# Kernel tuning notes

Hardware: AMD Instinct MI355X
Metric: run time of the kernel (lower is better)

Reference implementation:

```python
import jax, jax.numpy as jnp
import numpy as np

N = 4096        # nodes
C = 256         # in_channels
E0 = 65536      # edges before adding self-loops
RATIO = 0.5
K = int(np.ceil(RATIO * N))   # pooled nodes (topk)
NEG = 0.2       # leaky relu negative slope


def setup_inputs() -> dict:
    key = jax.random.key(0)
    ks = jax.random.split(key, 12)
    x = jax.random.normal(ks[0], (N, C), jnp.float32)
    src = jax.random.randint(ks[1], (E0,), 0, N)
    off = jax.random.randint(ks[2], (E0,), 1, N)
    dst = (src + off) % N                      # guaranteed no self-loops
    edge_index = jnp.stack([src, dst]).astype(jnp.int32)
    s = 1.0 / np.sqrt(C)
    s2 = 1.0 / np.sqrt(2 * C)
    u = lambda k, shape, b: jax.random.uniform(k, shape, jnp.float32, -b, b)
    return dict(
        x=x, edge_index=edge_index,
        Wq=u(ks[3], (C, C), s), bq=u(ks[4], (C,), s),          # lin_q
        gat_w=u(ks[5], (2 * C,), s2), gat_b=u(ks[6], (1,), s2),  # gat_att
        le1_w=u(ks[7], (C,), s), le1_b=u(ks[8], (1,), s),      # LEConv lin1
        le2_w=u(ks[9], (C,), s),                                # LEConv lin2 (no bias)
        le3_w=u(ks[10], (C,), s), le3_b=u(ks[11], (1,), s),    # LEConv lin3
    )


def _asap(x, edge_index, Wq, bq, gat_w, gat_b, le1_w, le1_b, le2_w, le3_w, le3_b):
    # add_remaining_self_loops (inputs have none -> all N loops, weight 1)
    loops = jnp.arange(N, dtype=edge_index.dtype)
    ei = jnp.concatenate([edge_index, jnp.stack([loops, loops])], axis=1)
    i, j = ei[0], ei[1]          # i: aggregation target, j: neighbor

    x_pool = x                   # GNN is None -> x_pool = x
    xj = x_pool[j]               # [E, C]

    # Master2Token attention: X_q = scatter_max over target i
    Xq = jax.ops.segment_max(xj, i, num_segments=N)       # [N, C]
    Mq = Xq @ Wq + bq                                     # lin_q
    sc = jnp.concatenate([Mq[i], xj], axis=-1) @ gat_w + gat_b[0]  # [E]
    sc = jnp.where(sc > 0, sc, NEG * sc)                  # leaky relu

    # segment softmax over targets i
    m = jax.ops.segment_max(sc, i, num_segments=N)
    e = jnp.exp(sc - m[i])
    z = jax.ops.segment_sum(e, i, num_segments=N)
    score = e / z[i]                                      # dropout_att=0, eval

    # cluster representation
    out = jax.ops.segment_sum(x[j] * score[:, None], i, num_segments=N)  # [N, C]

    # fitness = sigmoid(LEConv(out)): x_i' = lin3(x_i) + sum_j (lin1(x_j) - lin2(x_i))
    a = out @ le1_w + le1_b[0]                            # [N]
    b = out @ le2_w                                       # [N]
    agg = jax.ops.segment_sum(a[j] - b[i], i, num_segments=N)
    fitness = jax.nn.sigmoid(agg + out @ le3_w + le3_b[0])  # [N]

    # topk pooling (single graph -> global top_k)
    fit_k, perm = jax.lax.top_k(fitness, K)
    x_out = out[perm] * fit_k[:, None]                    # [K, C]

    # graph_connectivity: E = S^T A S (dense stand-in for coalesce+spspmm)
    n_idx = jnp.zeros(N, jnp.int32).at[perm].set(jnp.arange(K, dtype=jnp.int32))
    in_perm = jnp.zeros(N, bool).at[perm].set(True)
    sS = jax.lax.stop_gradient(score) * in_perm[i]        # score.detach(), kept-cluster edges
    S = jnp.zeros((N, K), x.dtype).at[j, n_idx[i]].add(sS)   # S[j, new(i)] = score
    A = jnp.zeros((N, N), x.dtype).at[i, j].add(1.0)      # edge_weight None -> ones, coalesced
    Eadj = S.T @ (A @ S)                                  # [K, K]
    # remove_self_loops then add_remaining_self_loops(fill=1)
    Eadj = Eadj - jnp.diag(jnp.diag(Eadj)) + jnp.eye(K, dtype=Eadj.dtype)
    return x_out, Eadj, perm


def reference(x, edge_index, Wq, bq, gat_w, gat_b, le1_w, le1_b, le2_w, le3_w, le3_b):
    return _asap(x, edge_index, Wq, bq, gat_w, gat_b,
                 le1_w, le1_b, le2_w, le3_w, le3_b)
```

## Files before the change

kernel.cpp:

```cpp
#include <hip/hip_runtime.h>
#include <math.h>

constexpr int NN  = 4096;
constexpr int CC  = 256;
constexpr int EE0 = 65536;
constexpr int EE  = 69632;
constexpr int KK  = 2048;
constexpr int SL  = 128;

__device__ __forceinline__ void edge_ij(const int* __restrict__ ei, int e, int& i, int& j) {
    if (e < EE0) { i = ei[e]; j = ei[EE0 + e]; }
    else         { i = e - EE0; j = i; }
}
__device__ __forceinline__ int edge_i(const int* __restrict__ ei, int e) {
    return (e < EE0) ? ei[e] : e - EE0;
}
__device__ __forceinline__ int edge_j(const int* __restrict__ ei, int e) {
    return (e < EE0) ? ei[EE0 + e] : e - EE0;
}

__global__ __launch_bounds__(256) void k_build(const int* __restrict__ ei,
                                               int* cnt_i, int* cnt_j,
                                               int* lst_i, int* lst_j,
                                               const float* __restrict__ x,
                                               const float* __restrict__ Wq, const float* __restrict__ bq,
                                               const float* __restrict__ gat_w, const float* __restrict__ gat_b,
                                               double* wv, double* consts, double* beta_node, int EB) {
    const int t = threadIdx.x, g = t >> 6, l = t & 63;
    if ((int)blockIdx.x < EB) {
        int e = blockIdx.x * 256 + t;
        if (e >= EE) return;
        int i, j; edge_ij(ei, e, i, j);
        int si = atomicAdd(&cnt_i[i], 1);
        lst_i[i * SL + si] = e;
        int sj = atomicAdd(&cnt_j[j], 1);
        lst_j[j * SL + sj] = e;
        return;
    }
    if ((int)blockIdx.x < EB + CC) {
        int k = blockIdx.x - EB;
        double s = (double)Wq[k * CC + t] * (double)gat_w[t];
        #pragma unroll
        for (int d = 32; d > 0; d >>= 1) s += __shfl_down(s, d, 64);
        __shared__ double red[4];
        if (l == 0) red[g] = s;
        __syncthreads();
        if (t == 0) wv[k] = red[0] + red[1] + red[2] + red[3];
        if (k == 0 && t == 0) {
            double cb = 0.0;
            for (int q = 0; q < CC; ++q) cb += (double)bq[q] * (double)gat_w[q];
            consts[0] = cb + (double)gat_b[0];
        }
        return;
    }
    int m = (blockIdx.x - EB - CC) * 4 + g;
    const float* gw2 = gat_w + CC;
    float4 v = ((const float4*)(x + (size_t)m * CC))[l];
    double s = (double)v.x * (double)gw2[4 * l]     + (double)v.y * (double)gw2[4 * l + 1]
             + (double)v.z * (double)gw2[4 * l + 2] + (double)v.w * (double)gw2[4 * l + 3];
    #pragma unroll
    for (int d = 32; d > 0; d >>= 1) s += __shfl_down(s, d, 64);
    if (l == 0) beta_node[m] = s;
}

__global__ __launch_bounds__(256) void k_attn(const float* __restrict__ x, const int* __restrict__ ei,
                                              const int* __restrict__ cnt_i, const int* __restrict__ lst_i,
                                              const int* __restrict__ cnt_j, const int* __restrict__ lst_j,
                                              const double* __restrict__ wv, const double* __restrict__ beta_node,
                                              const double* __restrict__ consts,
                                              const float* __restrict__ le1_w, const float* __restrict__ le1_b,
                                              const float* __restrict__ le2_w,
                                              const float* __restrict__ le3_w, const float* __restrict__ le3_b,
                                              float* __restrict__ score32, float* __restrict__ out32,
                                              double* __restrict__ zlog) {
    __shared__ int    sj[SL];
    __shared__ double ssc[SL];
    __shared__ double mz[2];
    __shared__ double bcast;
    __shared__ union { float4 m4[4][64]; double d[4][CC]; } red;

    const int n = blockIdx.x, t = threadIdx.x, g = t >> 6, l = t & 63;
    const int base = n * SL;
    const int deg = cnt_i[n];

    for (int p = t; p < deg; p += 256) {
        int e = lst_i[base + p];
        int j = edge_j(ei, e);
        sj[p] = j;
        ssc[p] = beta_node[j];
    }
    __syncthreads();

    float4 mx = make_float4(-INFINITY, -INFINITY, -INFINITY, -INFINITY);
    for (int p = g; p < deg; p += 4) {
        float4 v = ((const float4*)(x + (size_t)sj[p] * CC))[l];
        mx.x = fmaxf(mx.x, v.x); mx.y = fmaxf(mx.y, v.y);
        mx.z = fmaxf(mx.z, v.z); mx.w = fmaxf(mx.w, v.w);
    }
    red.m4[g][l] = mx;
    __syncthreads();
    if (g == 0) {
        float4 a = red.m4[0][l], b = red.m4[1][l], c2 = red.m4[2][l], d4 = red.m4[3][l];
        float m0 = fmaxf(fmaxf(a.x, b.x), fmaxf(c2.x, d4.x));
        float m1 = fmaxf(fmaxf(a.y, b.y), fmaxf(c2.y, d4.y));
        float m2 = fmaxf(fmaxf(a.z, b.z), fmaxf(c2.z, d4.z));
        float m3 = fmaxf(fmaxf(a.w, b.w), fmaxf(c2.w, d4.w));
        double alph = (double)m0 * wv[4 * l]     + (double)m1 * wv[4 * l + 1]
                    + (double)m2 * wv[4 * l + 2] + (double)m3 * wv[4 * l + 3];
        #pragma unroll
        for (int dd = 32; dd > 0; dd >>= 1) alph += __shfl_down(alph, dd, 64);
        if (l == 0) mz[0] = alph + consts[0];
    }
    __syncthreads();
    double an = mz[0];
    for (int p = t; p < deg; p += 256) {
        double v = an + ssc[p];
        ssc[p] = v > 0.0 ? v : 0.2 * v;
    }
    __syncthreads();
    if (t < 64) {
        double mm = -1e300;
        for (int p = l; p < deg; p += 64) mm = fmax(mm, ssc[p]);
        #pragma unroll
        for (int d = 32; d > 0; d >>= 1) mm = fmax(mm, __shfl_xor(mm, d, 64));
        double z = 0.0;
        for (int p = l; p < deg; p += 64) z += exp(ssc[p] - mm);
        #pragma unroll
        for (int d = 32; d > 0; d >>= 1) z += __shfl_xor(z, d, 64);
        if (l == 0) { mz[0] = mm; mz[1] = 1.0 / z; }
    }
    __syncthreads();
    double mm = mz[0], inv = mz[1];
    for (int p = t; p < deg; p += 256) {
        double sc = exp(ssc[p] - mm) * inv;
        ssc[p] = sc;
        score32[lst_i[base + p]] = (float)sc;
    }
    __syncthreads();
    double a0 = 0, a1 = 0, a2 = 0, a3 = 0;
    for (int p = g; p < deg; p += 4) {
        double sc = ssc[p];
        float4 v = ((const float4*)(x + (size_t)sj[p] * CC))[l];
        a0 += sc * (double)v.x; a1 += sc * (double)v.y;
        a2 += sc * (double)v.z; a3 += sc * (double)v.w;
    }
    red.d[g][4 * l + 0] = a0; red.d[g][4 * l + 1] = a1;
    red.d[g][4 * l + 2] = a2; red.d[g][4 * l + 3] = a3;
    __syncthreads();
    if (g == 0) {
        double o0 = red.d[0][4*l]   + red.d[1][4*l]   + red.d[2][4*l]   + red.d[3][4*l];
        double o1 = red.d[0][4*l+1] + red.d[1][4*l+1] + red.d[2][4*l+1] + red.d[3][4*l+1];
        double o2 = red.d[0][4*l+2] + red.d[1][4*l+2] + red.d[2][4*l+2] + red.d[3][4*l+2];
        double o3 = red.d[0][4*l+3] + red.d[1][4*l+3] + red.d[2][4*l+3] + red.d[3][4*l+3];
        float4 ov; ov.x = (float)o0; ov.y = (float)o1; ov.z = (float)o2; ov.w = (float)o3;
        ((float4*)(out32 + (size_t)n * CC))[l] = ov;
        float4 w1 = ((const float4*)le1_w)[l];
        float4 w2 = ((const float4*)le2_w)[l];
        float4 w3 = ((const float4*)le3_w)[l];
        double s1 = o0 * (double)w1.x + o1 * (double)w1.y + o2 * (double)w1.z + o3 * (double)w1.w;
        double s2 = o0 * (double)w2.x + o1 * (double)w2.y + o2 * (double)w2.z + o3 * (double)w2.w;
        double s3 = o0 * (double)w3.x + o1 * (double)w3.y + o2 * (double)w3.z + o3 * (double)w3.w;
        #pragma unroll
        for (int dd = 32; dd > 0; dd >>= 1) {
            s1 += __shfl_down(s1, dd, 64);
            s2 += __shfl_down(s2, dd, 64);
            s3 += __shfl_down(s3, dd, 64);
        }
        if (l == 0) {
            double a64n = s1 + (double)le1_b[0];
            double b64n = s2;
            double l3vn = s3 + (double)le3_b[0];
            atomicAdd(&zlog[n], l3vn - (double)deg * b64n);
            bcast = a64n;
        }
    }
    __syncthreads();
    double a64n = bcast;
    int cj = cnt_j[n], jb = n * SL;
    for (int p = t; p < cj; p += 256) {
        int e = lst_j[jb + p];
        atomicAdd(&zlog[edge_i(ei, e)], a64n);
    }
}

__global__ __launch_bounds__(256) void k_rank(const double* __restrict__ zlog,
                                              const float* __restrict__ out32,
                                              int* __restrict__ perm, int* __restrict__ n_idx,
                                              float* __restrict__ xout, float* __restrict__ operm) {
    int n = blockIdx.x, t = threadIdx.x;
    double zn = zlog[n];
    int cnt = 0;
    #pragma unroll
    for (int u = 0; u < NN / 256; ++u) {
        int m = t + u * 256;
        double zm = zlog[m];
        cnt += ((zm > zn) || (zm == zn && m < n)) ? 1 : 0;
    }
    #pragma unroll
    for (int d = 32; d > 0; d >>= 1) cnt += __shfl_down(cnt, d, 64);
    __shared__ int red[4];
    __shared__ int rr;
    if ((t & 63) == 0) red[t >> 6] = cnt;
    __syncthreads();
    if (t == 0) {
        int r = red[0] + red[1] + red[2] + red[3];
        rr = r;
        if (r < KK) {
            perm[r] = n;
            n_idx[n] = r;
            operm[r] = (float)n;
        } else {
            n_idx[n] = -1;
        }
    }
    __syncthreads();
    int r = rr;
    if (r < KK) {
        double fit = 1.0 / (1.0 + exp(-zn));
        xout[(size_t)r * CC + t] = (float)((double)out32[(size_t)n * CC + t] * fit);
    }
}

__global__ __launch_bounds__(256) void k_eadj(const int* __restrict__ ei,
                                              const int* __restrict__ cnt_i, const int* __restrict__ lst_i,
                                              const int* __restrict__ cnt_j, const int* __restrict__ lst_j,
                                              const int* __restrict__ n_idx,
                                              const int* __restrict__ perm,
                                              const float* __restrict__ score32,
                                              float* __restrict__ Ead) {
    __shared__ float row[KK];
    int r = blockIdx.x, t = threadIdx.x;
    float4 z4 = make_float4(0.f, 0.f, 0.f, 0.f);
    for (int c = t; c < KK / 4; c += 256) ((float4*)row)[c] = z4;
    __syncthreads();
    int n = perm[r];
    int deg = cnt_i[n];
    int base = n * SL;
    int grp = t >> 5, lane = t & 31;
    for (int p = grp; p < deg; p += 8) {
        int e = lst_i[base + p];
        float s1 = score32[e];
        int j = edge_j(ei, e);
        int cj = cnt_j[j], jb = j * SL;
        for (int q = lane; q < cj; q += 32) {
            int e2 = lst_j[jb + q];
            int c = n_idx[edge_i(ei, e2)];
            if (c >= 0) atomicAdd(&row[c], s1 * score32[e2]);
        }
    }
    __syncthreads();
    float* __restrict__ erow = Ead + (size_t)r * KK;
    for (int c4 = t; c4 < KK / 4; c4 += 256) {
        float4 v = ((float4*)row)[c4];
        int base4 = c4 * 4;
        int dr = r - base4;
        if (dr >= 0 && dr < 4) ((float*)&v)[dr] = 1.0f;
        ((float4*)erow)[c4] = v;
    }
}

extern "C" void kernel_launch(void* const* d_in, const int* in_sizes, int n_in,
                              void* d_out, int out_size, void* d_ws, size_t ws_size,
                              hipStream_t stream) {
    const float* x     = (const float*)d_in[0];
    const int*   ei    = (const int*)d_in[1];
    const float* Wq    = (const float*)d_in[2];
    const float* bq    = (const float*)d_in[3];
    const float* gat_w = (const float*)d_in[4];
    const float* gat_b = (const float*)d_in[5];
    const float* le1_w = (const float*)d_in[6];
    const float* le1_b = (const float*)d_in[7];
    const float* le2_w = (const float*)d_in[8];
    const float* le3_w = (const float*)d_in[9];
    const float* le3_b = (const float*)d_in[10];

    float* xout  = (float*)d_out;
    float* Ead   = xout + (size_t)KK * CC;
    float* operm = Ead + (size_t)KK * KK;

    char* w = (char*)d_ws;
    auto alloc = [&](size_t bytes) -> void* {
        void* p = (void*)w;
        w += (bytes + 255) & ~(size_t)255;
        return p;
    };
    int*    cnt_i  = (int*)alloc(NN * 4);
    int*    cnt_j  = (int*)alloc(NN * 4);
    double* zlog   = (double*)alloc(NN * 8);
    float*  score32= (float*)alloc(EE * 4);
    float*  out32  = (float*)alloc((size_t)NN * CC * 4);
    double* beta_node = (double*)alloc(NN * 8);
    double* wv     = (double*)alloc(CC * 8);
    double* consts = (double*)alloc(64);
    int* lst_i = (int*)alloc((size_t)NN * SL * 4);
    int* lst_j = (int*)alloc((size_t)NN * SL * 4);
    int* n_idx = (int*)alloc(NN * 4);
    int* perm  = (int*)alloc(KK * 4);

    hipMemsetAsync(cnt_i, 0, 2 * NN * 4 + NN * 8, stream);

    const int EB = (EE + 255) / 256;

    k_build<<<EB + CC + NN / 4, 256, 0, stream>>>(ei, cnt_i, cnt_j, lst_i, lst_j, x,
                                                  Wq, bq, gat_w, gat_b, wv, consts, beta_node, EB);
    k_attn<<<NN, 256, 0, stream>>>(x, ei, cnt_i, lst_i, cnt_j, lst_j, wv, beta_node, consts,
                                   le1_w, le1_b, le2_w, le3_w, le3_b,
                                   score32, out32, zlog);
    k_rank<<<NN, 256, 0, stream>>>(zlog, out32, perm, n_idx, xout, operm);
    k_eadj<<<KK, 256, 0, stream>>>(ei, cnt_i, lst_i, cnt_j, lst_j, n_idx, perm, score32, Ead);
}
```

Baseline: 155.4 us.

## Store neighbor ids and scores directly in CSR/CSC slot arrays

The adjacency lists now hold neighbor node ids instead of edge ids, plus a slot map from each target-side entry to its source-side position. Scores are written twice, once in target order and once in source order, so the Eadj two-hop loop reads contiguous score and neighbor arrays. This removes one level of indirection through edge_index and the scattered score32 gather in the hot loops. In exchange it adds a scattered store per edge in k_attn and more workspace memory.

```diff
diff --git a/kernel.cpp b/kernel.cpp
--- a/kernel.cpp
+++ b/kernel.cpp
@@ -12,16 +12,10 @@
     if (e < EE0) { i = ei[e]; j = ei[EE0 + e]; }
     else         { i = e - EE0; j = i; }
 }
-__device__ __forceinline__ int edge_i(const int* __restrict__ ei, int e) {
-    return (e < EE0) ? ei[e] : e - EE0;
-}
-__device__ __forceinline__ int edge_j(const int* __restrict__ ei, int e) {
-    return (e < EE0) ? ei[EE0 + e] : e - EE0;
-}
 
 __global__ __launch_bounds__(256) void k_build(const int* __restrict__ ei,
                                                int* cnt_i, int* cnt_j,
-                                               int* lst_i, int* lst_j,
+                                               int* lsti_j, int* slot_ij, int* lstj_i,
                                                const float* __restrict__ x,
                                                const float* __restrict__ Wq, const float* __restrict__ bq,
                                                const float* __restrict__ gat_w, const float* __restrict__ gat_b,
@@ -32,9 +26,10 @@
         if (e >= EE) return;
         int i, j; edge_ij(ei, e, i, j);
         int si = atomicAdd(&cnt_i[i], 1);
-        lst_i[i * SL + si] = e;
         int sj = atomicAdd(&cnt_j[j], 1);
-        lst_j[j * SL + sj] = e;
+        lsti_j[i * SL + si]  = j;
+        slot_ij[i * SL + si] = j * SL + sj;
+        lstj_i[j * SL + sj]  = i;
         return;
     }
     if ((int)blockIdx.x < EB + CC) {
@@ -63,15 +58,17 @@
     if (l == 0) beta_node[m] = s;
 }
 
-__global__ __launch_bounds__(256) void k_attn(const float* __restrict__ x, const int* __restrict__ ei,
-                                              const int* __restrict__ cnt_i, const int* __restrict__ lst_i,
-                                              const int* __restrict__ cnt_j, const int* __restrict__ lst_j,
+__global__ __launch_bounds__(256) void k_attn(const float* __restrict__ x,
+                                              const int* __restrict__ cnt_i, const int* __restrict__ lsti_j,
+                                              const int* __restrict__ slot_ij,
+                                              const int* __restrict__ cnt_j, const int* __restrict__ lstj_i,
                                               const double* __restrict__ wv, const double* __restrict__ beta_node,
                                               const double* __restrict__ consts,
                                               const float* __restrict__ le1_w, const float* __restrict__ le1_b,
                                               const float* __restrict__ le2_w,
                                               const float* __restrict__ le3_w, const float* __restrict__ le3_b,
-                                              float* __restrict__ score32, float* __restrict__ out32,
+                                              float* __restrict__ sval_i, float* __restrict__ svalj,
+                                              float* __restrict__ out32,
                                               double* __restrict__ zlog) {
     __shared__ int    sj[SL];
     __shared__ double ssc[SL];
@@ -84,8 +81,7 @@
     const int deg = cnt_i[n];
 
     for (int p = t; p < deg; p += 256) {
-        int e = lst_i[base + p];
-        int j = edge_j(ei, e);
+        int j = lsti_j[base + p];
         sj[p] = j;
         ssc[p] = beta_node[j];
     }
@@ -134,7 +130,9 @@
     for (int p = t; p < deg; p += 256) {
         double sc = exp(ssc[p] - mm) * inv;
         ssc[p] = sc;
-        score32[lst_i[base + p]] = (float)sc;
+        float scf = (float)sc;
+        sval_i[base + p] = scf;
+        svalj[slot_ij[base + p]] = scf;
     }
     __syncthreads();
     double a0 = 0, a1 = 0, a2 = 0, a3 = 0;
@@ -178,8 +176,7 @@
     double a64n = bcast;
     int cj = cnt_j[n], jb = n * SL;
     for (int p = t; p < cj; p += 256) {
-        int e = lst_j[jb + p];
-        atomicAdd(&zlog[edge_i(ei, e)], a64n);
+        atomicAdd(&zlog[lstj_i[jb + p]], a64n);
     }
 }
 
@@ -221,12 +218,12 @@
     }
 }
 
-__global__ __launch_bounds__(256) void k_eadj(const int* __restrict__ ei,
-                                              const int* __restrict__ cnt_i, const int* __restrict__ lst_i,
-                                              const int* __restrict__ cnt_j, const int* __restrict__ lst_j,
+__global__ __launch_bounds__(256) void k_eadj(const int* __restrict__ cnt_i, const int* __restrict__ lsti_j,
+                                              const float* __restrict__ sval_i,
+                                              const int* __restrict__ cnt_j, const int* __restrict__ lstj_i,
+                                              const float* __restrict__ svalj,
                                               const int* __restrict__ n_idx,
                                               const int* __restrict__ perm,
-                                              const float* __restrict__ score32,
                                               float* __restrict__ Ead) {
     __shared__ float row[KK];
     int r = blockIdx.x, t = threadIdx.x;
@@ -238,14 +235,12 @@
     int base = n * SL;
     int grp = t >> 5, lane = t & 31;
     for (int p = grp; p < deg; p += 8) {
-        int e = lst_i[base + p];
-        float s1 = score32[e];
-        int j = edge_j(ei, e);
+        int j = lsti_j[base + p];
+        float s1 = sval_i[base + p];
         int cj = cnt_j[j], jb = j * SL;
         for (int q = lane; q < cj; q += 32) {
-            int e2 = lst_j[jb + q];
-            int c = n_idx[edge_i(ei, e2)];
-            if (c >= 0) atomicAdd(&row[c], s1 * score32[e2]);
+            int c = n_idx[lstj_i[jb + q]];
+            if (c >= 0) atomicAdd(&row[c], s1 * svalj[jb + q]);
         }
     }
     __syncthreads();
@@ -287,25 +282,30 @@
     int*    cnt_i  = (int*)alloc(NN * 4);
     int*    cnt_j  = (int*)alloc(NN * 4);
     double* zlog   = (double*)alloc(NN * 8);
-    float*  score32= (float*)alloc(EE * 4);
     float*  out32  = (float*)alloc((size_t)NN * CC * 4);
     double* beta_node = (double*)alloc(NN * 8);
     double* wv     = (double*)alloc(CC * 8);
     double* consts = (double*)alloc(64);
-    int* lst_i = (int*)alloc((size_t)NN * SL * 4);
-    int* lst_j = (int*)alloc((size_t)NN * SL * 4);
-    int* n_idx = (int*)alloc(NN * 4);
-    int* perm  = (int*)alloc(KK * 4);
+    int*   lsti_j  = (int*)alloc((size_t)NN * SL * 4);
+    int*   slot_ij = (int*)alloc((size_t)NN * SL * 4);
+    int*   lstj_i  = (int*)alloc((size_t)NN * SL * 4);
+    float* sval_i  = (float*)alloc((size_t)NN * SL * 4);
+    float* svalj   = (float*)alloc((size_t)NN * SL * 4);
+    int*   n_idx   = (int*)alloc(NN * 4);
+    int*   perm    = (int*)alloc(KK * 4);
 
     hipMemsetAsync(cnt_i, 0, 2 * NN * 4 + NN * 8, stream);
 
     const int EB = (EE + 255) / 256;
 
-    k_build<<<EB + CC + NN / 4, 256, 0, stream>>>(ei, cnt_i, cnt_j, lst_i, lst_j, x,
+    k_build<<<EB + CC + NN / 4, 256, 0, stream>>>(ei, cnt_i, cnt_j,
+                                                  lsti_j, slot_ij, lstj_i, x,
                                                   Wq, bq, gat_w, gat_b, wv, consts, beta_node, EB);
-    k_attn<<<NN, 256, 0, stream>>>(x, ei, cnt_i, lst_i, cnt_j, lst_j, wv, beta_node, consts,
+    k_attn<<<NN, 256, 0, stream>>>(x, cnt_i, lsti_j, slot_ij, cnt_j, lstj_i,
+                                   wv, beta_node, consts,
                                    le1_w, le1_b, le2_w, le3_w, le3_b,
-                                   score32, out32, zlog);
+                                   sval_i, svalj, out32, zlog);
     k_rank<<<NN, 256, 0, stream>>>(zlog, out32, perm, n_idx, xout, operm);
-    k_eadj<<<KK, 256, 0, stream>>>(ei, cnt_i, lst_i, cnt_j, lst_j, n_idx, perm, score32, Ead);
-}
+    k_eadj<<<KK, 256, 0, stream>>>(cnt_i, lsti_j, sval_i, cnt_j, lstj_i, svalj,
+                                   n_idx, perm, Ead);
+}
```

Result: no change. 152.6 us (-1.8%).
